# Performance work log

Measured on AMD Instinct MI355X. Metric: run time of the kernel, lower is better.

The kernel has to match this reference:

```python
import jax, jax.numpy as jnp
import numpy as np

N_NODES = 100000
N_EDGES = 1600000
IN_DIM = 128
EMB_DIM = 32
K_HOPS = 3


def setup_inputs() -> dict:
    key = jax.random.key(0)
    k1, k2, k3, k4, k5, k6 = jax.random.split(key, 6)
    x = jax.random.normal(k1, (N_NODES, IN_DIM), dtype=jnp.float32)
    W = jax.random.normal(k2, (EMB_DIM, IN_DIM), dtype=jnp.float32) * (1.0 / np.sqrt(IN_DIM))
    b = jax.random.normal(k3, (EMB_DIM,), dtype=jnp.float32) * 0.01
    w = jax.random.uniform(k4, (N_EDGES,), dtype=jnp.float32)
    src = jax.random.randint(k5, (N_EDGES,), 0, N_NODES, dtype=jnp.int64)
    dst = jax.random.randint(k6, (N_EDGES,), 0, N_NODES, dtype=jnp.int64)
    return {"x": x, "W": W, "b": b, "w": w, "src": src, "dst": dst, "k": K_HOPS}


def reference(x, W, b, w, src, dst, k):
    # x: [N, in_dim] -> relu(linear) -> [N, emb_dim]
    h = jax.nn.relu(jnp.einsum("ni,ei->ne", x, W) + b)
    n_nodes = x.shape[0]
    # k hops of edge-weighted gather-multiply-scatter (u_mul_e / sum)
    for _ in range(k):
        msg = h[src] * w[:, None]              # [E, emb_dim]
        h = jax.ops.segment_sum(msg, dst, num_segments=n_nodes)
    return h
```

## Files before the change

### kernel.cpp

```cpp
#include <hip/hip_runtime.h>

constexpr int N_NODES_C = 100000;
constexpr int N_EDGES_C = 1600000;
constexpr int IN_DIM_C  = 128;
constexpr int EMB       = 32;

constexpr int SCAN_CHUNK  = 1024;
constexpr int SCAN_BLOCKS = (N_NODES_C + SCAN_CHUNK - 1) / SCAN_CHUNK;

__global__ __launch_bounds__(256) void linear_relu_kernel(
    const float* __restrict__ x, const float* __restrict__ W,
    const float* __restrict__ b, float* __restrict__ h, int n)
{
    int row = blockIdx.x * 256 + threadIdx.x;
    if (row >= n) return;
    const float4* __restrict__ xr =
        reinterpret_cast<const float4*>(x + (size_t)row * IN_DIM_C);
    const float4* __restrict__ W4 = reinterpret_cast<const float4*>(W);

    float acc[EMB];
#pragma unroll
    for (int e = 0; e < EMB; ++e) acc[e] = 0.f;

#pragma unroll 2
    for (int k4 = 0; k4 < IN_DIM_C / 4; ++k4) {
        float4 xv = xr[k4];
#pragma unroll
        for (int e = 0; e < EMB; ++e) {
            float4 wv = W4[e * (IN_DIM_C / 4) + k4];
            acc[e] = fmaf(xv.x, wv.x,
                     fmaf(xv.y, wv.y,
                     fmaf(xv.z, wv.z,
                     fmaf(xv.w, wv.w, acc[e]))));
        }
    }

    float* __restrict__ out = h + (size_t)row * EMB;
#pragma unroll
    for (int e = 0; e < EMB; ++e) {
        float v = acc[e] + b[e];
        out[e] = v > 0.f ? v : 0.f;
    }
}

__global__ __launch_bounds__(256) void hist_kernel(
    const int* __restrict__ dst, int* __restrict__ deg)
{
    int e = blockIdx.x * 256 + threadIdx.x;
    if (e < N_EDGES_C) atomicAdd(&deg[dst[e]], 1);
}

__global__ __launch_bounds__(256) void scan_phase_a(
    const int* __restrict__ deg, int* __restrict__ partial)
{
    int b = blockIdx.x, t = threadIdx.x;
    int base = b * SCAN_CHUNK + t * 4;
    int s = 0;
#pragma unroll
    for (int i = 0; i < 4; ++i)
        s += (base + i < N_NODES_C) ? deg[base + i] : 0;
#pragma unroll
    for (int ofs = 32; ofs >= 1; ofs >>= 1) s += __shfl_down(s, ofs, 64);
    __shared__ int wsum[4];
    int lane = t & 63, wid = t >> 6;
    if (lane == 0) wsum[wid] = s;
    __syncthreads();
    if (t == 0) partial[b] = wsum[0] + wsum[1] + wsum[2] + wsum[3];
}

__global__ void scan_phase_b(const int* __restrict__ partial,
                             int* __restrict__ block_base,
                             int* __restrict__ off)
{
    if (threadIdx.x == 0) {
        int run = 0;
        for (int i = 0; i < SCAN_BLOCKS; ++i) { block_base[i] = run; run += partial[i]; }
        off[N_NODES_C] = run;
    }
}

__global__ __launch_bounds__(256) void scan_phase_c(
    const int* __restrict__ deg, const int* __restrict__ block_base,
    int* __restrict__ off)
{
    int b = blockIdx.x, t = threadIdx.x;
    int base = b * SCAN_CHUNK + t * 4;
    int d[4];
#pragma unroll
    for (int i = 0; i < 4; ++i)
        d[i] = (base + i < N_NODES_C) ? deg[base + i] : 0;
    int tsum = d[0] + d[1] + d[2] + d[3];

    int lane = t & 63, wid = t >> 6;
    int v = tsum;
#pragma unroll
    for (int ofs = 1; ofs < 64; ofs <<= 1) {
        int u = __shfl_up(v, ofs, 64);
        if (lane >= ofs) v += u;
    }
    __shared__ int wsum[4];
    if (lane == 63) wsum[wid] = v;
    __syncthreads();
    int wofs = 0;
    for (int i = 0; i < wid; ++i) wofs += wsum[i];

    int gbase = block_base[b] + wofs + (v - tsum);
#pragma unroll
    for (int i = 0; i < 4; ++i) {
        if (base + i < N_NODES_C) off[base + i] = gbase;
        gbase += d[i];
    }
}

__global__ __launch_bounds__(256) void fill_kernel(
    const int* __restrict__ src, const int* __restrict__ dst,
    const float* __restrict__ w, const int* __restrict__ off,
    int* __restrict__ cur, int2* __restrict__ edge_pack)
{
    int e = blockIdx.x * 256 + threadIdx.x;
    if (e >= N_EDGES_C) return;
    int d = dst[e];
    int pos = off[d] + atomicAdd(&cur[d], 1);
    edge_pack[pos] = make_int2(src[e], __float_as_int(w[e]));
}

__global__ __launch_bounds__(256) void hop_csr_kernel(
    const float* __restrict__ h_in, const int* __restrict__ off,
    const int2* __restrict__ edge_pack, float* __restrict__ h_out)
{
    int tid = blockIdx.x * 256 + threadIdx.x;
    int node = tid >> 3;
    int q    = tid & 7;
    if (node >= N_NODES_C) return;

    int beg = off[node], end = off[node + 1];
    float4 acc = make_float4(0.f, 0.f, 0.f, 0.f);
    int j = beg;
    for (; j + 4 <= end; j += 4) {
        int2 ep0 = edge_pack[j + 0];
        int2 ep1 = edge_pack[j + 1];
        int2 ep2 = edge_pack[j + 2];
        int2 ep3 = edge_pack[j + 3];
        float4 h0 = *reinterpret_cast<const float4*>(h_in + (size_t)ep0.x * EMB + q * 4);
        float4 h1 = *reinterpret_cast<const float4*>(h_in + (size_t)ep1.x * EMB + q * 4);
        float4 h2 = *reinterpret_cast<const float4*>(h_in + (size_t)ep2.x * EMB + q * 4);
        float4 h3 = *reinterpret_cast<const float4*>(h_in + (size_t)ep3.x * EMB + q * 4);
        float w0 = __int_as_float(ep0.y), w1 = __int_as_float(ep1.y);
        float w2 = __int_as_float(ep2.y), w3 = __int_as_float(ep3.y);
        acc.x = fmaf(h0.x, w0, acc.x); acc.y = fmaf(h0.y, w0, acc.y);
        acc.z = fmaf(h0.z, w0, acc.z); acc.w = fmaf(h0.w, w0, acc.w);
        acc.x = fmaf(h1.x, w1, acc.x); acc.y = fmaf(h1.y, w1, acc.y);
        acc.z = fmaf(h1.z, w1, acc.z); acc.w = fmaf(h1.w, w1, acc.w);
        acc.x = fmaf(h2.x, w2, acc.x); acc.y = fmaf(h2.y, w2, acc.y);
        acc.z = fmaf(h2.z, w2, acc.z); acc.w = fmaf(h2.w, w2, acc.w);
        acc.x = fmaf(h3.x, w3, acc.x); acc.y = fmaf(h3.y, w3, acc.y);
        acc.z = fmaf(h3.z, w3, acc.z); acc.w = fmaf(h3.w, w3, acc.w);
    }
    for (; j < end; ++j) {
        int2  ep = edge_pack[j];
        float wt = __int_as_float(ep.y);
        float4 hv = *reinterpret_cast<const float4*>(
            h_in + (size_t)ep.x * EMB + q * 4);
        acc.x = fmaf(hv.x, wt, acc.x);
        acc.y = fmaf(hv.y, wt, acc.y);
        acc.z = fmaf(hv.z, wt, acc.z);
        acc.w = fmaf(hv.w, wt, acc.w);
    }
    *reinterpret_cast<float4*>(h_out + (size_t)node * EMB + q * 4) = acc;
}

extern "C" void kernel_launch(void* const* d_in, const int* in_sizes, int n_in,
                              void* d_out, int out_size, void* d_ws, size_t ws_size,
                              hipStream_t stream) {
    const float* x   = (const float*)d_in[0];
    const float* W   = (const float*)d_in[1];
    const float* b   = (const float*)d_in[2];
    const float* w   = (const float*)d_in[3];
    const int*   src = (const int*)d_in[4];
    const int*   dst = (const int*)d_in[5];

    float* out = (float*)d_out;

    char* ws = (char*)d_ws;
    size_t o = 0;
    auto alloc = [&](size_t bytes) {
        char* p = ws + o;
        o += (bytes + 255) & ~(size_t)255;
        return p;
    };
    float* h0        = (float*)alloc((size_t)N_NODES_C * EMB * sizeof(float));
    int*   deg       = (int*)  alloc((size_t)N_NODES_C * sizeof(int));
    int*   off       = (int*)  alloc((size_t)(N_NODES_C + 1) * sizeof(int));
    int*   cur       = (int*)  alloc((size_t)N_NODES_C * sizeof(int));
    int*   partial   = (int*)  alloc((size_t)SCAN_BLOCKS * sizeof(int));
    int*   blockbase = (int*)  alloc((size_t)SCAN_BLOCKS * sizeof(int));
    int2*  edge_pack = (int2*) alloc((size_t)N_EDGES_C * sizeof(int2));

    const int EB = (N_EDGES_C + 255) / 256;
    const int HB = (N_NODES_C * 8 + 255) / 256;

    hipMemsetAsync(deg, 0, (size_t)N_NODES_C * sizeof(int), stream);
    hist_kernel<<<EB, 256, 0, stream>>>(dst, deg);
    scan_phase_a<<<SCAN_BLOCKS, 256, 0, stream>>>(deg, partial);
    scan_phase_b<<<1, 64, 0, stream>>>(partial, blockbase, off);
    scan_phase_c<<<SCAN_BLOCKS, 256, 0, stream>>>(deg, blockbase, off);
    hipMemsetAsync(cur, 0, (size_t)N_NODES_C * sizeof(int), stream);
    fill_kernel<<<EB, 256, 0, stream>>>(src, dst, w, off, cur, edge_pack);

    linear_relu_kernel<<<(N_NODES_C + 255) / 256, 256, 0, stream>>>(
        x, W, b, h0, N_NODES_C);

    hop_csr_kernel<<<HB, 256, 0, stream>>>(h0, off, edge_pack, out);
    hop_csr_kernel<<<HB, 256, 0, stream>>>(out, off, edge_pack, h0);
    hop_csr_kernel<<<HB, 256, 0, stream>>>(h0, off, edge_pack, out);
}
```

Measured before the change: 426.9 us.

## Build CSR via two-level bucket sort with striped coarse counters

Replaces the per-node histogram, three-phase scan and per-node atomic fill with a coarse two-level counting sort. Edges are first bucketed by 64-node groups using 8 counter columns striped by block index to spread atomic contention, scanned in a single block, then each group is locally sorted in shared memory to produce per-node offsets. This cuts kernel launches and global atomic contention, at the cost of an extra pass over the edge records and packing the low destination bits into the source index, which assumes node ids fit in 17 bits.

Measured after the change: 439.1 us. 2.9% more time.

```diff
diff --git a/kernel.cpp b/kernel.cpp
--- a/kernel.cpp
+++ b/kernel.cpp
@@ -5,8 +5,11 @@
 constexpr int IN_DIM_C  = 128;
 constexpr int EMB       = 32;
 
-constexpr int SCAN_CHUNK  = 1024;
-constexpr int SCAN_BLOCKS = (N_NODES_C + SCAN_CHUNK - 1) / SCAN_CHUNK;
+constexpr int NPB   = 64;
+constexpr int NB    = (N_NODES_C + NPB - 1) / NPB;
+constexpr int NCOL  = 8;
+constexpr int NCNT  = NB * NCOL;
+constexpr int SCAN_PER = (NCNT + 255) / 256;
 
 __global__ __launch_bounds__(256) void linear_relu_kernel(
     const float* __restrict__ x, const float* __restrict__ W,
@@ -43,104 +46,115 @@
     }
 }
 
-__global__ __launch_bounds__(256) void hist_kernel(
-    const int* __restrict__ dst, int* __restrict__ deg)
+__global__ __launch_bounds__(256) void hist8_kernel(
+    const int* __restrict__ dst, int* __restrict__ cnt8)
 {
     int e = blockIdx.x * 256 + threadIdx.x;
-    if (e < N_EDGES_C) atomicAdd(&deg[dst[e]], 1);
-}
-
-__global__ __launch_bounds__(256) void scan_phase_a(
-    const int* __restrict__ deg, int* __restrict__ partial)
-{
-    int b = blockIdx.x, t = threadIdx.x;
-    int base = b * SCAN_CHUNK + t * 4;
+    if (e < N_EDGES_C)
+        atomicAdd(&cnt8[(dst[e] >> 6) * NCOL + (blockIdx.x & 7)], 1);
+}
+
+__global__ __launch_bounds__(256) void scan12k_kernel(
+    const int* __restrict__ cnt8, int* __restrict__ boff8, int* __restrict__ cur8)
+{
+    int t = threadIdx.x;
+    int base = t * SCAN_PER;
+    int v[SCAN_PER];
     int s = 0;
 #pragma unroll
-    for (int i = 0; i < 4; ++i)
-        s += (base + i < N_NODES_C) ? deg[base + i] : 0;
-#pragma unroll
-    for (int ofs = 32; ofs >= 1; ofs >>= 1) s += __shfl_down(s, ofs, 64);
-    __shared__ int wsum[4];
+    for (int i = 0; i < SCAN_PER; ++i) {
+        int x = (base + i < NCNT) ? cnt8[base + i] : 0;
+        v[i] = x; s += x;
+    }
     int lane = t & 63, wid = t >> 6;
-    if (lane == 0) wsum[wid] = s;
-    __syncthreads();
-    if (t == 0) partial[b] = wsum[0] + wsum[1] + wsum[2] + wsum[3];
-}
-
-__global__ void scan_phase_b(const int* __restrict__ partial,
-                             int* __restrict__ block_base,
-                             int* __restrict__ off)
-{
-    if (threadIdx.x == 0) {
-        int run = 0;
-        for (int i = 0; i < SCAN_BLOCKS; ++i) { block_base[i] = run; run += partial[i]; }
-        off[N_NODES_C] = run;
-    }
-}
-
-__global__ __launch_bounds__(256) void scan_phase_c(
-    const int* __restrict__ deg, const int* __restrict__ block_base,
-    int* __restrict__ off)
-{
-    int b = blockIdx.x, t = threadIdx.x;
-    int base = b * SCAN_CHUNK + t * 4;
-    int d[4];
-#pragma unroll
-    for (int i = 0; i < 4; ++i)
-        d[i] = (base + i < N_NODES_C) ? deg[base + i] : 0;
-    int tsum = d[0] + d[1] + d[2] + d[3];
-
-    int lane = t & 63, wid = t >> 6;
-    int v = tsum;
-#pragma unroll
-    for (int ofs = 1; ofs < 64; ofs <<= 1) {
-        int u = __shfl_up(v, ofs, 64);
-        if (lane >= ofs) v += u;
-    }
-    __shared__ int wsum[4];
-    if (lane == 63) wsum[wid] = v;
-    __syncthreads();
-    int wofs = 0;
-    for (int i = 0; i < wid; ++i) wofs += wsum[i];
-
-    int gbase = block_base[b] + wofs + (v - tsum);
-#pragma unroll
-    for (int i = 0; i < 4; ++i) {
-        if (base + i < N_NODES_C) off[base + i] = gbase;
-        gbase += d[i];
-    }
-}
-
-__global__ __launch_bounds__(256) void fill_kernel(
+    int inc = s;
+#pragma unroll
+    for (int o = 1; o < 64; o <<= 1) {
+        int u = __shfl_up(inc, o, 64);
+        if (lane >= o) inc += u;
+    }
+    __shared__ int wtot[4];
+    if (lane == 63) wtot[wid] = inc;
+    __syncthreads();
+    int wbase = 0;
+    for (int i = 0; i < wid; ++i) wbase += wtot[i];
+    int run = wbase + inc - s;
+#pragma unroll
+    for (int i = 0; i < SCAN_PER; ++i) {
+        if (base + i < NCNT) { boff8[base + i] = run; cur8[base + i] = 0; }
+        run += v[i];
+    }
+    if (t == 255) boff8[NCNT] = run;
+}
+
+__global__ __launch_bounds__(256) void cfill_kernel(
     const int* __restrict__ src, const int* __restrict__ dst,
-    const float* __restrict__ w, const int* __restrict__ off,
-    int* __restrict__ cur, int2* __restrict__ edge_pack)
+    const float* __restrict__ w, const int* __restrict__ boff8,
+    int* __restrict__ cur8, int2* __restrict__ recs)
 {
     int e = blockIdx.x * 256 + threadIdx.x;
     if (e >= N_EDGES_C) return;
-    int d = dst[e];
-    int pos = off[d] + atomicAdd(&cur[d], 1);
-    edge_pack[pos] = make_int2(src[e], __float_as_int(w[e]));
+    int d   = dst[e];
+    int idx = (d >> 6) * NCOL + (blockIdx.x & 7);
+    int pos = boff8[idx] + atomicAdd(&cur8[idx], 1);
+    recs[pos] = make_int2(src[e] | ((d & 63) << 17), __float_as_int(w[e]));
+}
+
+__global__ __launch_bounds__(256) void sort_kernel(
+    const int2* __restrict__ recs, const int* __restrict__ boff8,
+    int2* __restrict__ recs2, int* __restrict__ nodeoff)
+{
+    __shared__ int hist[NPB];
+    __shared__ int pfx[NPB];
+    __shared__ int cur[NPB];
+    int t = threadIdx.x;
+    int b = blockIdx.x;
+    if (t < NPB) { hist[t] = 0; cur[t] = 0; }
+    __syncthreads();
+
+    int beg = boff8[b * NCOL];
+    int end = boff8[(b + 1) * NCOL];
+
+    for (int j = beg + t; j < end; j += 256)
+        atomicAdd(&hist[(recs[j].x >> 17) & 63], 1);
+    __syncthreads();
+
+    if (t == 0) {
+        int run = 0;
+        for (int i = 0; i < NPB; ++i) { pfx[i] = run; run += hist[i]; }
+    }
+    __syncthreads();
+
+    if (t < NPB) {
+        int node = b * NPB + t;
+        if (node <= N_NODES_C) nodeoff[node] = beg + pfx[t];
+    }
+
+    for (int j = beg + t; j < end; j += 256) {
+        int2 r = recs[j];
+        int dlow = (r.x >> 17) & 63;
+        int pos  = beg + pfx[dlow] + atomicAdd(&cur[dlow], 1);
+        recs2[pos] = make_int2(r.x & 0x1FFFF, r.y);
+    }
 }
 
 __global__ __launch_bounds__(256) void hop_csr_kernel(
-    const float* __restrict__ h_in, const int* __restrict__ off,
-    const int2* __restrict__ edge_pack, float* __restrict__ h_out)
+    const float* __restrict__ h_in, const int* __restrict__ nodeoff,
+    const int2* __restrict__ recs2, float* __restrict__ h_out)
 {
     int tid = blockIdx.x * 256 + threadIdx.x;
     int node = tid >> 3;
     int q    = tid & 7;
     if (node >= N_NODES_C) return;
 
-    int beg = off[node], end = off[node + 1];
+    int beg = nodeoff[node], end = nodeoff[node + 1];
     float4 acc = make_float4(0.f, 0.f, 0.f, 0.f);
     int j = beg;
     for (; j + 4 <= end; j += 4) {
-        int2 ep0 = edge_pack[j + 0];
-        int2 ep1 = edge_pack[j + 1];
-        int2 ep2 = edge_pack[j + 2];
-        int2 ep3 = edge_pack[j + 3];
+        int2 ep0 = recs2[j + 0];
+        int2 ep1 = recs2[j + 1];
+        int2 ep2 = recs2[j + 2];
+        int2 ep3 = recs2[j + 3];
         float4 h0 = *reinterpret_cast<const float4*>(h_in + (size_t)ep0.x * EMB + q * 4);
         float4 h1 = *reinterpret_cast<const float4*>(h_in + (size_t)ep1.x * EMB + q * 4);
         float4 h2 = *reinterpret_cast<const float4*>(h_in + (size_t)ep2.x * EMB + q * 4);
@@ -157,10 +171,9 @@
         acc.z = fmaf(h3.z, w3, acc.z); acc.w = fmaf(h3.w, w3, acc.w);
     }
     for (; j < end; ++j) {
-        int2  ep = edge_pack[j];
+        int2  ep = recs2[j];
         float wt = __int_as_float(ep.y);
-        float4 hv = *reinterpret_cast<const float4*>(
-            h_in + (size_t)ep.x * EMB + q * 4);
+        float4 hv = *reinterpret_cast<const float4*>(h_in + (size_t)ep.x * EMB + q * 4);
         acc.x = fmaf(hv.x, wt, acc.x);
         acc.y = fmaf(hv.y, wt, acc.y);
         acc.z = fmaf(hv.z, wt, acc.z);
@@ -188,29 +201,27 @@
         o += (bytes + 255) & ~(size_t)255;
         return p;
     };
-    float* h0        = (float*)alloc((size_t)N_NODES_C * EMB * sizeof(float));
-    int*   deg       = (int*)  alloc((size_t)N_NODES_C * sizeof(int));
-    int*   off       = (int*)  alloc((size_t)(N_NODES_C + 1) * sizeof(int));
-    int*   cur       = (int*)  alloc((size_t)N_NODES_C * sizeof(int));
-    int*   partial   = (int*)  alloc((size_t)SCAN_BLOCKS * sizeof(int));
-    int*   blockbase = (int*)  alloc((size_t)SCAN_BLOCKS * sizeof(int));
-    int2*  edge_pack = (int2*) alloc((size_t)N_EDGES_C * sizeof(int2));
+    float* h0      = (float*)alloc((size_t)N_NODES_C * EMB * sizeof(float));
+    int*   cnt8    = (int*)  alloc((size_t)NCNT * sizeof(int));
+    int*   boff8   = (int*)  alloc((size_t)(NCNT + 1) * sizeof(int));
+    int*   cur8    = (int*)  alloc((size_t)NCNT * sizeof(int));
+    int*   nodeoff = (int*)  alloc((size_t)(N_NODES_C + 1) * sizeof(int));
+    int2*  recs    = (int2*) alloc((size_t)N_EDGES_C * sizeof(int2));
+    int2*  recs2   = (int2*) alloc((size_t)N_EDGES_C * sizeof(int2));
 
     const int EB = (N_EDGES_C + 255) / 256;
     const int HB = (N_NODES_C * 8 + 255) / 256;
 
-    hipMemsetAsync(deg, 0, (size_t)N_NODES_C * sizeof(int), stream);
-    hist_kernel<<<EB, 256, 0, stream>>>(dst, deg);
-    scan_phase_a<<<SCAN_BLOCKS, 256, 0, stream>>>(deg, partial);
-    scan_phase_b<<<1, 64, 0, stream>>>(partial, blockbase, off);
-    scan_phase_c<<<SCAN_BLOCKS, 256, 0, stream>>>(deg, blockbase, off);
-    hipMemsetAsync(cur, 0, (size_t)N_NODES_C * sizeof(int), stream);
-    fill_kernel<<<EB, 256, 0, stream>>>(src, dst, w, off, cur, edge_pack);
+    hipMemsetAsync(cnt8, 0, (size_t)NCNT * sizeof(int), stream);
+    hist8_kernel<<<EB, 256, 0, stream>>>(dst, cnt8);
+    scan12k_kernel<<<1, 256, 0, stream>>>(cnt8, boff8, cur8);
+    cfill_kernel<<<EB, 256, 0, stream>>>(src, dst, w, boff8, cur8, recs);
+    sort_kernel<<<NB, 256, 0, stream>>>(recs, boff8, recs2, nodeoff);
 
     linear_relu_kernel<<<(N_NODES_C + 255) / 256, 256, 0, stream>>>(
         x, W, b, h0, N_NODES_C);
 
-    hop_csr_kernel<<<HB, 256, 0, stream>>>(h0, off, edge_pack, out);
-    hop_csr_kernel<<<HB, 256, 0, stream>>>(out, off, edge_pack, h0);
-    hop_csr_kernel<<<HB, 256, 0, stream>>>(h0, off, edge_pack, out);
-}
+    hop_csr_kernel<<<HB, 256, 0, stream>>>(h0, nodeoff, recs2, out);
+    hop_csr_kernel<<<HB, 256, 0, stream>>>(out, nodeoff, recs2, h0);
+    hop_csr_kernel<<<HB, 256, 0, stream>>>(h0, nodeoff, recs2, out);
+}
```
